# Kernel tuning notes

Hardware: AMD Instinct MI355X
Metric: run time of the kernel (lower is better)

The kernel has to match this reference:

```python
import jax, jax.numpy as jnp
import numpy as np

L, C, S = 4096, 128, 64
SAMPLE_RATE = 4096.0  # Hz; dt offset is 1/sample_rate as in the flax module


def setup_inputs() -> dict:
    key = jax.random.key(0)
    ks = jax.random.split(key, 4)
    x = jax.random.normal(ks[0], (L, C), dtype=jnp.float32)
    # S4D-real init: A = -arange(1, S+1), param stores log(-A) broadcast to (C, S)
    A_log = jnp.broadcast_to(
        jnp.log(jnp.arange(1, S + 1, dtype=jnp.float32)), (C, S)
    )
    sc = 1.0 / np.sqrt(C)  # lecun_normal-like scale for Dense kernels
    B_kernel = (jax.random.normal(ks[1], (C, S)) * sc).astype(jnp.float32)
    B_bias = jnp.zeros((S,), jnp.float32)
    C_kernel = (jax.random.normal(ks[2], (C, S)) * sc).astype(jnp.float32)
    C_bias = jnp.zeros((S,), jnp.float32)
    dt_kernel = (jax.random.normal(ks[3], (C, C)) * sc).astype(jnp.float32)
    dt_bias = jnp.zeros((C,), jnp.float32)
    return {
        "x": x,
        "A_log": A_log,
        "B_kernel": B_kernel,
        "B_bias": B_bias,
        "C_kernel": C_kernel,
        "C_bias": C_bias,
        "dt_kernel": dt_kernel,
        "dt_bias": dt_bias,
    }


def reference(x, A_log, B_kernel, B_bias, C_kernel, C_bias, dt_kernel, dt_bias):
    # ssm params
    A = -jnp.exp(A_log)                                   # (C, S), negative real
    B = 1.0 + x @ B_kernel + B_bias                       # (L, S)
    Cm = x @ C_kernel + C_bias                            # (L, S)
    dt = jax.nn.softplus(1.0 / SAMPLE_RATE + x @ dt_kernel + dt_bias)  # (L, C)
    # discretization (ZOH for diagonal real A)
    At = jnp.exp(A[None, :, :] * dt[:, :, None])          # (L, C, S)
    ut = (At - 1.0) * (B[:, None, :] / A[None, :, :]) * x[:, :, None]  # (L, C, S)

    # parallel linear-recurrence scan: h_t = At_t * h_{t-1} + ut_t, h0 = 0
    def comb(e1, e2):
        a1, u1 = e1
        a2, u2 = e2
        return (a2 * a1, a2 * u1 + u2)

    _, ht = jax.lax.associative_scan(comb, (At, ut))      # scans over axis 0 (L)
    y = jnp.einsum("ls,lcs->lc", Cm, ht)                  # (L, C)
    return y
```

## Files before the change

kernel.cpp:

```cpp
#include <hip/hip_runtime.h>
#include <math.h>

#define LL 4096
#define CC 128
#define SS 64
#define CLEN 32
#define GW 8
#define NG 16
#define CS 8192
#define LOG2E 1.44269504088896f

__global__ __launch_bounds__(512) void k_proj(
    const float* __restrict__ x,
    const float* __restrict__ Bk, const float* __restrict__ Bb,
    const float* __restrict__ Ck, const float* __restrict__ Cb,
    const float* __restrict__ Dk, const float* __restrict__ Db,
    float* __restrict__ Bmat, float* __restrict__ Cmat,
    float* __restrict__ DTmT, float* __restrict__ xT)
{
    __shared__ float xs[CC][20];
    const int r0 = blockIdx.x * 16;
    const int t = threadIdx.x;
    {
        const int r = t >> 5, k4 = (t & 31) * 4;
        const float4 v = *(const float4*)&x[(r0 + r) * CC + k4];
        xs[k4+0][r] = v.x; xs[k4+1][r] = v.y; xs[k4+2][r] = v.z; xs[k4+3][r] = v.w;
    }
    __syncthreads();
    {
        const int k = t >> 2, q = (t & 3) * 4;
        *(float4*)&xT[k * LL + r0 + q] = *(const float4*)&xs[k][q];
    }
    const int tc = t & 63, tr = t >> 6;
    const int rb = r0 + 2 * tr;
    const float* Wb; int wstride, wo;
    if (tc < 16)      { Wb = Bk; wstride = SS; wo = 4 * tc; }
    else if (tc < 32) { Wb = Ck; wstride = SS; wo = 4 * tc - 64; }
    else              { Wb = Dk; wstride = CC; wo = 4 * tc - 128; }
    float acc[2][4];
#pragma unroll
    for (int r = 0; r < 2; ++r)
#pragma unroll
        for (int j = 0; j < 4; ++j) acc[r][j] = 0.0f;
    for (int k = 0; k < CC; ++k) {
        const float4 wq = *(const float4*)(Wb + k * wstride + wo);
        const float2 xq = *(const float2*)&xs[k][2 * tr];
        const float wv[4] = {wq.x, wq.y, wq.z, wq.w};
        const float xv[2] = {xq.x, xq.y};
#pragma unroll
        for (int r = 0; r < 2; ++r)
#pragma unroll
            for (int j = 0; j < 4; ++j) acc[r][j] = fmaf(xv[r], wv[j], acc[r][j]);
    }
    if (tc < 32) {
        const float* bb = (tc < 16) ? Bb : Cb;
        const float add = (tc < 16) ? 1.0f : 0.0f;
        float bias[4];
#pragma unroll
        for (int j = 0; j < 4; ++j) bias[j] = add + bb[wo + j];
        float* dst = (tc < 16) ? Bmat : Cmat;
#pragma unroll
        for (int r = 0; r < 2; ++r) {
            const float4 o = make_float4(acc[r][0] + bias[0], acc[r][1] + bias[1],
                                         acc[r][2] + bias[2], acc[r][3] + bias[3]);
            *(float4*)&dst[(rb + r) * SS + wo] = o;
        }
    } else {
#pragma unroll
        for (int j = 0; j < 4; ++j) {
            const float bj = Db[wo + j] + 0.000244140625f;
            float sp[2];
#pragma unroll
            for (int r = 0; r < 2; ++r) {
                const float z = acc[r][j] + bj;
                sp[r] = fmaxf(z, 0.0f) + log1pf(__expf(-fabsf(z)));
            }
            *(float2*)&DTmT[(wo + j) * LL + rb] = make_float2(sp[0], sp[1]);
        }
    }
}

__global__ __launch_bounds__(512, 4) void k_sweep1(
    const float* __restrict__ xT, const float* __restrict__ A_log,
    const float* __restrict__ Bmat, const float* __restrict__ DTmT,
    float2* __restrict__ GaGu)
{
    __shared__ float2 agg[GW][SS];
    const int lane = threadIdx.x & 63;
    const int w = __builtin_amdgcn_readfirstlane(threadIdx.x >> 6);
    const int c = blockIdx.x >> 4;
    const int g = blockIdx.x & (NG - 1);
    const int j = c * SS + lane;
    const float A = -__expf(A_log[j]);
    const float A2 = A * LOG2E;
    const float invA = 1.0f / A;
    const int l0 = (g * GW + w) * CLEN;
    const float* dtp = DTmT + c * LL + l0;
    const float* xp  = xT   + c * LL + l0;
    const float* Bp  = Bmat + l0 * SS + lane;
    float ap = 1.0f, uc = 0.0f;
#pragma unroll
    for (int i = 0; i < CLEN; ++i) {
        const float At = __builtin_amdgcn_exp2f(A2 * dtp[i]);
        const float u  = (At - 1.0f) * invA * (Bp[i * SS] * xp[i]);
        ap *= At;
        uc = fmaf(At, uc, u);
    }
    agg[w][lane] = make_float2(ap, uc);
    __syncthreads();
    if (w == 0) {
        float ga = 1.0f, gu = 0.0f;
#pragma unroll
        for (int k = 0; k < GW; ++k) {
            const float2 t = agg[k][lane];
            gu = fmaf(t.x, gu, t.y);
            ga *= t.x;
        }
        GaGu[g * CS + j] = make_float2(ga, gu);
    }
}

__global__ __launch_bounds__(512, 2) void k_emit(
    const float* __restrict__ xT, const float* __restrict__ A_log,
    const float* __restrict__ Bmat, const float* __restrict__ Cmat,
    const float* __restrict__ DTmT,
    const float2* __restrict__ GaGu,
    float* __restrict__ y)
{
    __shared__ float2 agg[GW][SS];
    __shared__ float hgs[SS];
    const int lane = threadIdx.x & 63;
    const int w = __builtin_amdgcn_readfirstlane(threadIdx.x >> 6);
    const int c = blockIdx.x >> 4;
    const int g = blockIdx.x & (NG - 1);
    const int j = c * SS + lane;
    const float A = -__expf(A_log[j]);
    const float A2 = A * LOG2E;
    const float invA = 1.0f / A;
    if (w == 0) {
        float hg = 0.0f;
        float2 ggr[NG - 1];
#pragma unroll
        for (int gg = 0; gg < NG - 1; ++gg) ggr[gg] = GaGu[gg * CS + j];
#pragma unroll
        for (int gg = 0; gg < NG - 1; ++gg)
            hg = (gg < g) ? fmaf(ggr[gg].x, hg, ggr[gg].y) : hg;
        hgs[lane] = hg;
    }
    const int l0 = (g * GW + w) * CLEN;
    const float* dtp = DTmT + c * LL + l0;
    const float* xp  = xT   + c * LL + l0;
    const float* Bp  = Bmat + l0 * SS + lane;
    const float* Cp  = Cmat + l0 * SS + lane;
    float at[CLEN], uu[CLEN];
    {
        float ap = 1.0f, uc = 0.0f;
#pragma unroll
        for (int i = 0; i < CLEN; ++i) {
            at[i] = __builtin_amdgcn_exp2f(A2 * dtp[i]);
            uu[i] = (at[i] - 1.0f) * invA * (Bp[i * SS] * xp[i]);
            ap *= at[i];
            uc = fmaf(at[i], uc, uu[i]);
        }
        agg[w][lane] = make_float2(ap, uc);
    }
    __syncthreads();
    const float hg = hgs[lane];
    float ea = 1.0f, eu = 0.0f;
    for (int k = 0; k < w; ++k) {
        const float2 t = agg[k][lane];
        eu = fmaf(t.x, eu, t.y);
        ea *= t.x;
    }
    float h = fmaf(ea, hg, eu);
#pragma unroll
    for (int i = 0; i < CLEN; ++i) {
        h = fmaf(at[i], h, uu[i]);
        uu[i] = Cp[i * SS] * h;
    }
#pragma unroll
    for (int k = 0; k < 5; ++k) {
        const int d = 1 << k;
        const bool hi = (lane & d) != 0;
#pragma unroll
        for (int i2 = 0; i2 < (CLEN >> (k + 1)); ++i2) {
            const float a = uu[2 * i2], b = uu[2 * i2 + 1];
            const float send = hi ? a : b;
            const float t = __shfl_xor(send, d, 64);
            uu[i2] = (hi ? b : a) + t;
        }
    }
    const float t = __shfl_xor(uu[0], 32, 64);
    const float yv = uu[0] + t;
    if (lane < 32) y[(l0 + lane) * CC + c] = yv;
}

extern "C" void kernel_launch(void* const* d_in, const int* in_sizes, int n_in,
                              void* d_out, int out_size, void* d_ws, size_t ws_size,
                              hipStream_t stream)
{
    const float* x  = (const float*)d_in[0];
    const float* Al = (const float*)d_in[1];
    const float* Bk = (const float*)d_in[2];
    const float* Bb = (const float*)d_in[3];
    const float* Ck = (const float*)d_in[4];
    const float* Cb = (const float*)d_in[5];
    const float* Dk = (const float*)d_in[6];
    const float* Db = (const float*)d_in[7];
    float* y  = (float*)d_out;
    float* ws = (float*)d_ws;

    float*  Bmat = ws;
    float*  Cmat = Bmat + LL * SS;
    float*  DTmT = Cmat + LL * SS;
    float*  xT   = DTmT + CC * LL;
    float2* GaGu = (float2*)(xT + CC * LL);

    k_proj  <<<LL / 16, 512, 0, stream>>>(x, Bk, Bb, Ck, Cb, Dk, Db, Bmat, Cmat, DTmT, xT);
    k_sweep1<<<CC * NG, 512, 0, stream>>>(xT, Al, Bmat, DTmT, GaGu);
    k_emit  <<<CC * NG, 512, 0, stream>>>(xT, Al, Bmat, Cmat, DTmT, GaGu, y);
}
```

Baseline: 54.08 us.

## Split projection kernel into two half-blocks and batch weight loads; raise emit occupancy

The projection kernel now launches twice as many 256-thread blocks. One half computes the B/C projections and the other computes dt plus the x transpose, which spreads the GEMM work over more CUs. Weight loads are batched eight k-steps at a time to expose more memory-level parallelism. The emit kernel's launch bounds are raised to 4 blocks per SM, which caps registers and risks spilling its 64-entry per-thread arrays.

```diff
diff --git a/kernel.cpp b/kernel.cpp
--- a/kernel.cpp
+++ b/kernel.cpp
@@ -10,7 +10,7 @@
 #define CS 8192
 #define LOG2E 1.44269504088896f
 
-__global__ __launch_bounds__(512) void k_proj(
+__global__ __launch_bounds__(256) void k_proj(
     const float* __restrict__ x,
     const float* __restrict__ Bk, const float* __restrict__ Bb,
     const float* __restrict__ Ck, const float* __restrict__ Cb,
@@ -19,46 +19,61 @@
     float* __restrict__ DTmT, float* __restrict__ xT)
 {
     __shared__ float xs[CC][20];
-    const int r0 = blockIdx.x * 16;
+    const int stripe = blockIdx.x >> 1;
+    const int h = blockIdx.x & 1;
+    const int r0 = stripe * 16;
     const int t = threadIdx.x;
     {
-        const int r = t >> 5, k4 = (t & 31) * 4;
-        const float4 v = *(const float4*)&x[(r0 + r) * CC + k4];
-        xs[k4+0][r] = v.x; xs[k4+1][r] = v.y; xs[k4+2][r] = v.z; xs[k4+3][r] = v.w;
+        const int r = t >> 4, k8 = (t & 15) * 8;
+        const float4 v0 = *(const float4*)&x[(r0 + r) * CC + k8];
+        const float4 v1 = *(const float4*)&x[(r0 + r) * CC + k8 + 4];
+        xs[k8+0][r] = v0.x; xs[k8+1][r] = v0.y; xs[k8+2][r] = v0.z; xs[k8+3][r] = v0.w;
+        xs[k8+4][r] = v1.x; xs[k8+5][r] = v1.y; xs[k8+6][r] = v1.z; xs[k8+7][r] = v1.w;
     }
     __syncthreads();
-    {
-        const int k = t >> 2, q = (t & 3) * 4;
-        *(float4*)&xT[k * LL + r0 + q] = *(const float4*)&xs[k][q];
-    }
-    const int tc = t & 63, tr = t >> 6;
+    const int tc = t & 31;
+    const int tr = t >> 5;
     const int rb = r0 + 2 * tr;
-    const float* Wb; int wstride, wo;
-    if (tc < 16)      { Wb = Bk; wstride = SS; wo = 4 * tc; }
-    else if (tc < 32) { Wb = Ck; wstride = SS; wo = 4 * tc - 64; }
-    else              { Wb = Dk; wstride = CC; wo = 4 * tc - 128; }
+    const float* W; int wstr, wo;
+    bool isB = false;
+    if (h == 0) {
+        isB = (tc < 16);
+        if (isB) { W = Bk; wstr = SS; wo = 4 * tc; }
+        else     { W = Ck; wstr = SS; wo = 4 * tc - 64; }
+    } else       { W = Dk; wstr = CC; wo = 4 * tc; }
+
     float acc[2][4];
 #pragma unroll
     for (int r = 0; r < 2; ++r)
 #pragma unroll
         for (int j = 0; j < 4; ++j) acc[r][j] = 0.0f;
-    for (int k = 0; k < CC; ++k) {
-        const float4 wq = *(const float4*)(Wb + k * wstride + wo);
-        const float2 xq = *(const float2*)&xs[k][2 * tr];
-        const float wv[4] = {wq.x, wq.y, wq.z, wq.w};
-        const float xv[2] = {xq.x, xq.y};
-#pragma unroll
-        for (int r = 0; r < 2; ++r)
-#pragma unroll
-            for (int j = 0; j < 4; ++j) acc[r][j] = fmaf(xv[r], wv[j], acc[r][j]);
-    }
-    if (tc < 32) {
-        const float* bb = (tc < 16) ? Bb : Cb;
-        const float add = (tc < 16) ? 1.0f : 0.0f;
+
+    for (int k0 = 0; k0 < CC; k0 += 8) {
+        float4 wq[8];
+#pragma unroll
+        for (int i = 0; i < 8; ++i)
+            wq[i] = *(const float4*)(W + (k0 + i) * wstr + wo);
+#pragma unroll
+        for (int i = 0; i < 8; ++i) {
+            const float2 xq = *(const float2*)&xs[k0 + i][2 * tr];
+            acc[0][0] = fmaf(xq.x, wq[i].x, acc[0][0]);
+            acc[0][1] = fmaf(xq.x, wq[i].y, acc[0][1]);
+            acc[0][2] = fmaf(xq.x, wq[i].z, acc[0][2]);
+            acc[0][3] = fmaf(xq.x, wq[i].w, acc[0][3]);
+            acc[1][0] = fmaf(xq.y, wq[i].x, acc[1][0]);
+            acc[1][1] = fmaf(xq.y, wq[i].y, acc[1][1]);
+            acc[1][2] = fmaf(xq.y, wq[i].z, acc[1][2]);
+            acc[1][3] = fmaf(xq.y, wq[i].w, acc[1][3]);
+        }
+    }
+
+    if (h == 0) {
+        const float* bb = isB ? Bb : Cb;
+        const float add = isB ? 1.0f : 0.0f;
+        float* dst = isB ? Bmat : Cmat;
         float bias[4];
 #pragma unroll
         for (int j = 0; j < 4; ++j) bias[j] = add + bb[wo + j];
-        float* dst = (tc < 16) ? Bmat : Cmat;
 #pragma unroll
         for (int r = 0; r < 2; ++r) {
             const float4 o = make_float4(acc[r][0] + bias[0], acc[r][1] + bias[1],
@@ -77,6 +92,11 @@
             }
             *(float2*)&DTmT[(wo + j) * LL + rb] = make_float2(sp[0], sp[1]);
         }
+        const int k = t >> 1, half8 = (t & 1) * 8;
+        const float4 a = *(const float4*)&xs[k][half8];
+        const float4 b = *(const float4*)&xs[k][half8 + 4];
+        *(float4*)&xT[k * LL + r0 + half8]     = a;
+        *(float4*)&xT[k * LL + r0 + half8 + 4] = b;
     }
 }
 
@@ -120,7 +140,7 @@
     }
 }
 
-__global__ __launch_bounds__(512, 2) void k_emit(
+__global__ __launch_bounds__(512, 4) void k_emit(
     const float* __restrict__ xT, const float* __restrict__ A_log,
     const float* __restrict__ Bmat, const float* __restrict__ Cmat,
     const float* __restrict__ DTmT,
@@ -216,7 +236,7 @@
     float*  xT   = DTmT + CC * LL;
     float2* GaGu = (float2*)(xT + CC * LL);
 
-    k_proj  <<<LL / 16, 512, 0, stream>>>(x, Bk, Bb, Ck, Cb, Dk, Db, Bmat, Cmat, DTmT, xT);
-    k_sweep1<<<CC * NG, 512, 0, stream>>>(xT, Al, Bmat, DTmT, GaGu);
-    k_emit  <<<CC * NG, 512, 0, stream>>>(xT, Al, Bmat, Cmat, DTmT, GaGu, y);
-}
+    k_proj  <<<2 * (LL / 16), 256, 0, stream>>>(x, Bk, Bb, Ck, Cb, Dk, Db, Bmat, Cmat, DTmT, xT);
+    k_sweep1<<<CC * NG,       512, 0, stream>>>(xT, Al, Bmat, DTmT, GaGu);
+    k_emit  <<<CC * NG,       512, 0, stream>>>(xT, Al, Bmat, Cmat, DTmT, GaGu, y);
+}
```

Result: faster. 47.72 us (-11.8%).
